# Performance work log

Hardware: AMD Instinct MI355X
Metric: run time of the kernel (lower is better)

The kernel has to match this reference:

```python
import jax, jax.numpy as jnp
import numpy as np
from jax import lax

NUM_CLASSES = 21      # VOC: background (class 0) + 20 fg classes
TOP_K = 200           # max detections kept per (image, class)
CONF_THRESH = 0.01
NMS_THRESH = 0.45
VAR0, VAR1 = 0.1, 0.2 # cfg.VARIANCE
K_PRE = 256           # candidates pre-selected per class before NMS (fixed-shape NMS)


def setup_inputs() -> dict:
    key = jax.random.key(0)
    k1, k2, k3 = jax.random.split(key, 3)
    B, P, C = 32, 8732, NUM_CLASSES
    loc_data = jax.random.normal(k1, (B, P, 4), dtype=jnp.float32)
    conf_data = jax.random.normal(k2, (B, P, C), dtype=jnp.float32)
    u = jax.random.uniform(k3, (P, 4), dtype=jnp.float32)
    # priors in center-offset form: centers in [0,1), w/h in [0.02, 0.32)
    prior_data = jnp.concatenate([u[:, :2], 0.02 + 0.3 * u[:, 2:]], axis=-1)
    return {"loc_data": loc_data, "conf_data": conf_data, "prior_data": prior_data}


def decode(loc, priors):
    # loc, priors: [..., 4]; priors are (cx, cy, w, h)
    centers = priors[..., :2] + loc[..., :2] * VAR0 * priors[..., 2:]
    wh = priors[..., 2:] * jnp.exp(loc[..., 2:] * VAR1)
    xy_min = centers - wh * 0.5
    return jnp.concatenate([xy_min, xy_min + wh], axis=-1)  # (x1,y1,x2,y2)


def pairwise_iou(b):
    # b: [K, 4] corner boxes -> [K, K] IoU
    area = jnp.maximum(b[:, 2] - b[:, 0], 0.0) * jnp.maximum(b[:, 3] - b[:, 1], 0.0)
    lt = jnp.maximum(b[:, None, :2], b[None, :, :2])
    rb = jnp.minimum(b[:, None, 2:], b[None, :, 2:])
    wh = jnp.clip(rb - lt, 0.0)
    inter = wh[..., 0] * wh[..., 1]
    union = area[:, None] + area[None, :] - inter
    return inter / jnp.maximum(union, 1e-9)


def nms_one_class(scores_p, boxes_p4):
    # scores_p: [P], boxes_p4: [P, 4]; fixed-shape NMS -> [TOP_K, 5] (score, x1, y1, x2, y2)
    vals, idx = lax.top_k(scores_p, K_PRE)          # sorted descending
    cand = boxes_p4[idx]                            # [K_PRE, 4]
    valid = vals > CONF_THRESH
    iou = pairwise_iou(cand)                        # [K_PRE, K_PRE]
    ar = jnp.arange(K_PRE)

    def step(keep, i):
        # a kept box suppresses later boxes overlapping it above threshold
        sup = keep[i] & (iou[i] > NMS_THRESH) & (ar > i)
        return keep & (~sup), None

    keep, _ = lax.scan(step, valid, ar)
    kept_scores = jnp.where(keep, vals, 0.0)
    # kept entries are already score-ordered; pull the top TOP_K survivors to the front
    sv, si = lax.top_k(kept_scores, TOP_K)
    out_boxes = jnp.where(sv[:, None] > 0.0, cand[si], 0.0)
    return jnp.concatenate([sv[:, None], out_boxes], axis=-1)  # [TOP_K, 5]


def reference(loc_data, conf_data, prior_data):
    # loc_data: [B, P, 4], conf_data: [B, P, C], prior_data: [P, 4]
    probs = jax.nn.softmax(conf_data, axis=-1)                     # [B, P, C]
    probs_fg = jnp.swapaxes(probs[..., 1:], 1, 2)                  # [B, C-1, P] (skip background)
    boxes = decode(loc_data, prior_data[None, :, :])               # [B, P, 4]
    # vmap over classes, then over batch
    per_class = jax.vmap(nms_one_class, in_axes=(0, None))         # ([C-1,P],[P,4]) -> [C-1,TOP_K,5]
    per_image = jax.vmap(per_class, in_axes=(0, 0))
    return per_image(probs_fg, boxes)                              # [B, C-1, TOP_K, 5]
```

## Files before the change

### kernel.cpp

```cpp
#include <hip/hip_runtime.h>
#include <stdint.h>

typedef unsigned long long ull;
typedef float f4v __attribute__((ext_vector_type(4)));

#define NUM_CLASSES 21
#define NFG 20
#define TOPK 200
#define KPRE 256
#define CONF_TH 0.01f
#define NMS_TH 0.45f
#define VAR0 0.1f
#define VAR1 0.2f
#define NVMAX 35
#define BITS_CONF 0x3C23D70Au
#define BSLOT(g) ((g) + ((g) >> 6))

__global__ __launch_bounds__(256) void softmax_probs_kernel(
    const float* __restrict__ conf, float* __restrict__ probs, int B, int P) {
    __shared__ __align__(16) float buf[256 * NUM_CLASSES];
    const int t = threadIdx.x;
    const int nch = (P + 255) >> 8;

    const int id = blockIdx.x;
    int b, chk;
    if ((B & 7) == 0) {
        int r = id & 7, m = id >> 3;
        int q = m / nch;
        b = r + (q << 3);
        chk = m - q * nch;
    } else {
        b = id / nch;
        chk = id - b * nch;
    }
    const int p0 = chk << 8;
    const int cnt = min(256, P - p0);
    const float* src = conf + ((size_t)b * P + p0) * NUM_CLASSES;

    if (cnt == 256) {
        const f4v* s4 = (const f4v*)src;
        f4v* b4 = (f4v*)buf;
#pragma unroll
        for (int k = 0; k < 6; ++k) {
            int i = (k << 8) + t;
            if (i < (256 * NUM_CLASSES) / 4)
                b4[i] = __builtin_nontemporal_load(s4 + i);
        }
    } else {
        int n = cnt * NUM_CLASSES;
        for (int i = t; i < n; i += 256) buf[i] = src[i];
    }
    __syncthreads();

    float sc[NFG];
    if (t < cnt) {
        const float* row = buf + t * NUM_CLASSES;
        float x[NUM_CLASSES];
        float mx = row[0];
        x[0] = mx;
#pragma unroll
        for (int j = 1; j < NUM_CLASSES; ++j) { x[j] = row[j]; mx = fmaxf(mx, x[j]); }
        float s = 0.f;
#pragma unroll
        for (int j = 0; j < NUM_CLASSES; ++j) { x[j] = expf(x[j] - mx); s += x[j]; }
#pragma unroll
        for (int c = 1; c < NUM_CLASSES; ++c)
            sc[c - 1] = x[c] / s;
    }
    __syncthreads();

    if (t < cnt) {
#pragma unroll
        for (int c = 0; c < NFG; ++c)
            buf[c * 256 + t] = sc[c];
    }
    __syncthreads();

    float* dst = probs + ((size_t)b * NFG) * P + p0;
    if (cnt == 256) {
#pragma unroll
        for (int k = 0; k < 5; ++k) {
            int e = (k << 8) + t;
            int c = e >> 6;
            int f = e & 63;
            f4v val = ((const f4v*)buf)[(c << 6) + f];
            __builtin_nontemporal_store(val, (f4v*)(dst + (size_t)c * P + (f << 2)));
        }
    } else {
        for (int e = t; e < NFG * cnt; e += 256) {
            int c = e / cnt;
            int f = e - c * cnt;
            __builtin_nontemporal_store(buf[c * 256 + f], dst + (size_t)c * P + f);
        }
    }
}

__global__ __launch_bounds__(KPRE) void nms_topk_kernel(
    const float* __restrict__ probs, const float* __restrict__ loc,
    const float* __restrict__ prior, float* __restrict__ out, int B, int P) {

    __shared__ ull arr[2 * KPRE];
    __shared__ ull arr2[2 * KPRE];
    __shared__ int wsum[2][4];
    __shared__ int s_cnt;
    __shared__ float4 sbox[KPRE + (KPRE >> 6)];
    __shared__ float sarea[KPRE + (KPRE >> 6)];
    __shared__ ull smask[KPRE][5];
    __shared__ ull kept_mask[4];

    const int t = threadIdx.x;
    const int lane = t & 63;
    const int wid = t >> 6;
    const ull lmask_lt = (1ULL << lane) - 1ULL;

    const int g = blockIdx.x;
    int b, c;
    if ((B & 7) == 0) {
        int k = g >> 3;
        b = ((k / NFG) << 3) + (g & 7);
        c = k - (k / NFG) * NFG;
    } else {
        b = g / NFG;
        c = g - (g / NFG) * NFG;
    }
    const int pair = b * NFG + c;
    const float* sp = probs + (size_t)pair * P;

    unsigned int ubits[NVMAX];
#pragma unroll
    for (int i = 0; i < NVMAX; ++i) {
        int p = (i << 8) + t;
        ubits[i] = (p < P) ? __float_as_uint(sp[p]) : 0u;
    }

    {
        unsigned int lo = 0x3C23u, hi = 0x3F81u;
        while (hi - lo > 1u) {
            unsigned int mid = lo + ((hi - lo) >> 1);
            unsigned int m32 = mid << 16;
            int cc = 0;
#pragma unroll
            for (int i = 0; i < NVMAX; ++i)
                cc += __popcll(__ballot(ubits[i] >= m32));
            if (cc >= KPRE / 4) lo = mid; else hi = mid;
        }
        if (lane == 0) wsum[0][wid] = (int)(lo << 16);
    }
    __syncthreads();
    unsigned int T = (unsigned int)min(min(wsum[0][0], wsum[0][1]),
                                       min(wsum[0][2], wsum[0][3]));

    int nval;
    for (int attempt = 0;; ++attempt) {
        if (t == 0) s_cnt = 0;
        __syncthreads();
        int wtot = 0;
#pragma unroll
        for (int i = 0; i < NVMAX; ++i) {
            int p = (i << 8) + t;
            bool pred = (p < P) && (ubits[i] >= T);
            wtot += __popcll(__ballot(pred));
        }
        int wbase = 0;
        if (lane == 0) wbase = atomicAdd(&s_cnt, wtot);
        wbase = __shfl(wbase, 0);
        int run = wbase;
#pragma unroll
        for (int i = 0; i < NVMAX; ++i) {
            int p = (i << 8) + t;
            bool pred = (p < P) && (ubits[i] >= T);
            ull bal = __ballot(pred);
            if (pred) {
                int slot = run + __popcll(bal & lmask_lt);
                if (slot < 2 * KPRE)
                    arr[slot] = ((ull)ubits[i] << 32) | (unsigned int)(~p);
            }
            run += __popcll(bal);
        }
        __syncthreads();
        if (s_cnt <= 2 * KPRE || attempt == 1) { nval = min(s_cnt, 2 * KPRE); break; }
        unsigned int lo = T, hi = 0x3F800001u;
        int it = 0;
        while (hi - lo > 1u) {
            unsigned int mid = lo + ((hi - lo) >> 1);
            int cc = 0;
#pragma unroll
            for (int i = 0; i < NVMAX; ++i)
                cc += __popcll(__ballot(ubits[i] >= mid));
            if (lane == 0) wsum[it & 1][wid] = cc;
            __syncthreads();
            int totc = wsum[it & 1][0] + wsum[it & 1][1] + wsum[it & 1][2] + wsum[it & 1][3];
            if (totc >= KPRE) lo = mid; else hi = mid;
            ++it;
        }
        T = lo;
    }

    for (int e = t; e < 2 * KPRE; e += KPRE)
        if (e >= nval) arr[e] = 0ULL;
    __syncthreads();

    ull k0 = arr[t];
    ull k1 = arr[t + KPRE];
    {
        int lstage = 0;
#pragma unroll
        for (int kk = 2; kk <= 2 * KPRE; kk <<= 1) {
#pragma unroll
            for (int j = kk >> 1; j > 0; j >>= 1) {
                if (j == KPRE) {
                    ull mx = (k0 > k1) ? k0 : k1;
                    ull mn = (k0 > k1) ? k1 : k0;
                    k0 = mx; k1 = mn;
                } else if (j >= 64) {
                    ull* A = (lstage & 1) ? arr : arr2;
                    ++lstage;
                    A[t] = k0; A[t + KPRE] = k1;
                    __syncthreads();
                    ull o0 = A[t ^ j];
                    ull o1 = A[(t + KPRE) ^ j];
                    bool amLow = ((t & j) == 0);
                    bool d0 = ((t & kk) == 0);
                    bool d1 = (((t + KPRE) & kk) == 0);
                    k0 = (d0 == amLow) ? ((k0 > o0) ? k0 : o0) : ((k0 > o0) ? o0 : k0);
                    k1 = (d1 == amLow) ? ((k1 > o1) ? k1 : o1) : ((k1 > o1) ? o1 : k1);
                } else {
                    ull o0 = __shfl_xor(k0, j);
                    ull o1 = __shfl_xor(k1, j);
                    bool amLow = ((t & j) == 0);
                    bool d0 = ((t & kk) == 0);
                    bool d1 = (((t + KPRE) & kk) == 0);
                    k0 = (d0 == amLow) ? ((k0 > o0) ? k0 : o0) : ((k0 > o0) ? o0 : k0);
                    k1 = (d1 == amLow) ? ((k1 > o1) ? k1 : o1) : ((k1 > o1) ? o1 : k1);
                }
            }
        }
    }
    const ull key = k0;

    float v = __uint_as_float((unsigned int)(key >> 32));
    int idx = (int)(~(unsigned int)(key & 0xFFFFFFFFu));
    if (idx < 0 || idx >= P) { idx = 0; v = 0.f; }

    const float4 lv = *(const float4*)(loc + ((size_t)b * P + idx) * 4);
    const float4 pv = *(const float4*)(prior + (size_t)idx * 4);
    float cx = pv.x + (lv.x * VAR0) * pv.z;
    float cy = pv.y + (lv.y * VAR0) * pv.w;
    float w = pv.z * expf(lv.z * VAR1);
    float h = pv.w * expf(lv.w * VAR1);
    float x1 = cx - w * 0.5f;
    float y1 = cy - h * 0.5f;
    float x2 = x1 + w;
    float y2 = y1 + h;
    float myarea = fmaxf(x2 - x1, 0.f) * fmaxf(y2 - y1, 0.f);

    sbox[BSLOT(t)] = make_float4(x1, y1, x2, y2);
    sarea[BSLOT(t)] = myarea;
    __syncthreads();

#pragma unroll
    for (int rep = 0; rep < 3; ++rep) {
        int pid = t + (rep << 8);
        if (pid < 640) {
            int r, w2;
            if (pid < 64)       { r = pid;                w2 = 0; }
            else if (pid < 192) { int q = pid - 64;  r = 64  + (q >> 1); w2 = q & 1; }
            else if (pid < 384) { int q = pid - 192; int q3 = q / 3; r = 128 + q3; w2 = q - 3 * q3; }
            else                { int q = pid - 384; r = 192 + (q >> 2); w2 = q & 3; }
            float4 rb = sbox[BSLOT(r)];
            float ra = sarea[BSLOT(r)];
            ull mm = 0ULL;
            for (int i = 0; i < 64; ++i) {
                int gg = (w2 << 6) + i;
                float4 gb = sbox[BSLOT(gg)];
                float lx = fmaxf(gb.x, rb.x), ly = fmaxf(gb.y, rb.y);
                float rx = fminf(gb.z, rb.z), ry = fminf(gb.w, rb.w);
                float iw = fmaxf(rx - lx, 0.f), ih = fmaxf(ry - ly, 0.f);
                float inter = iw * ih;
                float uni = sarea[BSLOT(gg)] + ra - inter;
                bool s = (inter / fmaxf(uni, 1e-9f)) > NMS_TH;
                mm |= ((ull)(s ? 1u : 0u)) << i;
            }
            smask[r][w2] = mm;
        }
    }
    __syncthreads();

    ull m0 = smask[t][0];
    ull m1 = (wid >= 1) ? smask[t][1] : 0ULL;
    ull m2 = (wid >= 2) ? smask[t][2] : 0ULL;
    ull m3 = (wid >= 3) ? smask[t][3] : 0ULL;
    if (wid == 0) m0 &= lmask_lt;
    else if (wid == 1) m1 &= lmask_lt;
    else if (wid == 2) m2 &= lmask_lt;
    else m3 &= lmask_lt;

    int alive = (v > CONF_TH) ? 1 : 0;
    ull mykept = 0ULL;
#pragma unroll
    for (int w2 = 0; w2 < 4; ++w2) {
        if (wid == w2) {
            if (w2 > 0 && (m0 & kept_mask[0])) alive = 0;
            if (w2 > 1 && (m1 & kept_mask[1])) alive = 0;
            if (w2 > 2 && (m2 & kept_mask[2])) alive = 0;
            ull mw = (w2 == 0) ? m0 : (w2 == 1) ? m1 : (w2 == 2) ? m2 : m3;
            ull validb = __ballot(alive != 0);
            ull todo = __ballot((mw & validb) != 0ULL) & validb;
            ull kept = validb & ~todo;
            while (todo) {
                int i = __builtin_ctzll(todo);
                ull row = __shfl(mw, i);
                if ((row & kept) == 0ULL) kept |= (1ULL << i);
                todo &= (todo - 1ULL);
            }
            mykept = kept;
            alive = (int)((kept >> lane) & 1ULL);
            if (lane == 0) kept_mask[w2] = kept;
        }
        __syncthreads();
    }

    int rank = 0;
#pragma unroll
    for (int w2 = 0; w2 < 4; ++w2)
        if (w2 < wid) rank += __popcll(kept_mask[w2]);
    rank += __popcll(mykept & lmask_lt);
    int total = 0;
#pragma unroll
    for (int w2 = 0; w2 < 4; ++w2) total += __popcll(kept_mask[w2]);

    float* orow = out + (size_t)pair * TOPK * 5;
    if (alive && rank < TOPK) {
        float* o = orow + rank * 5;
        o[0] = v; o[1] = x1; o[2] = y1; o[3] = x2; o[4] = y2;
    }
    if (t < TOPK && t >= total) {
        float* o = orow + t * 5;
        o[0] = 0.f; o[1] = 0.f; o[2] = 0.f; o[3] = 0.f; o[4] = 0.f;
    }
}

extern "C" void kernel_launch(void* const* d_in, const int* in_sizes, int n_in,
                              void* d_out, int out_size, void* d_ws, size_t ws_size,
                              hipStream_t stream) {
    const float* loc = (const float*)d_in[0];
    const float* conf = (const float*)d_in[1];
    const float* prior = (const float*)d_in[2];
    float* out = (float*)d_out;
    float* probs = (float*)d_ws;

    int P = in_sizes[2] / 4;
    int B = in_sizes[0] / (4 * P);
    int nch = (P + 255) / 256;

    softmax_probs_kernel<<<dim3(B * nch), 256, 0, stream>>>(conf, probs, B, P);
    nms_topk_kernel<<<B * NFG, KPRE, 0, stream>>>(probs, loc, prior, out, B, P);
}
```

Measured before the change: 130.4 us.

## Store truncated 16-bit probabilities and recompute exact scores for candidates only

```diff
diff --git a/kernel.cpp b/kernel.cpp
--- a/kernel.cpp
+++ b/kernel.cpp
@@ -12,13 +12,16 @@
 #define NMS_TH 0.45f
 #define VAR0 0.1f
 #define VAR1 0.2f
-#define NVMAX 35
-#define BITS_CONF 0x3C23D70Au
+#define NV16 18
+#define T16_LO 0x3C23u
+#define T16_HI 0x3F81u
 #define BSLOT(g) ((g) + ((g) >> 6))
 
-__global__ __launch_bounds__(256) void softmax_probs_kernel(
-    const float* __restrict__ conf, float* __restrict__ probs, int B, int P) {
+__global__ __launch_bounds__(256) void rownorm16_kernel(
+    const float* __restrict__ conf, float2* __restrict__ norm,
+    ushort* __restrict__ probs16, int B, int P) {
     __shared__ __align__(16) float buf[256 * NUM_CLASSES];
+    __shared__ __align__(16) ushort b16[NFG * 256];
     const int t = threadIdx.x;
     const int nch = (P + 255) >> 8;
 
@@ -43,8 +46,7 @@
 #pragma unroll
         for (int k = 0; k < 6; ++k) {
             int i = (k << 8) + t;
-            if (i < (256 * NUM_CLASSES) / 4)
-                b4[i] = __builtin_nontemporal_load(s4 + i);
+            if (i < (256 * NUM_CLASSES) / 4) b4[i] = s4[i];
         }
     } else {
         int n = cnt * NUM_CLASSES;
@@ -52,7 +54,6 @@
     }
     __syncthreads();
 
-    float sc[NFG];
     if (t < cnt) {
         const float* row = buf + t * NUM_CLASSES;
         float x[NUM_CLASSES];
@@ -63,40 +64,37 @@
         float s = 0.f;
 #pragma unroll
         for (int j = 0; j < NUM_CLASSES; ++j) { x[j] = expf(x[j] - mx); s += x[j]; }
-#pragma unroll
-        for (int c = 1; c < NUM_CLASSES; ++c)
-            sc[c - 1] = x[c] / s;
-    }
-    __syncthreads();
-
-    if (t < cnt) {
-#pragma unroll
-        for (int c = 0; c < NFG; ++c)
-            buf[c * 256 + t] = sc[c];
-    }
-    __syncthreads();
-
-    float* dst = probs + ((size_t)b * NFG) * P + p0;
+        norm[(size_t)b * P + p0 + t] = make_float2(mx, s);
+#pragma unroll
+        for (int c = 1; c < NUM_CLASSES; ++c) {
+            float v = x[c] / s;
+            b16[(c - 1) * 256 + t] = (ushort)(__float_as_uint(v) >> 16);
+        }
+    }
+    __syncthreads();
+
     if (cnt == 256) {
-#pragma unroll
-        for (int k = 0; k < 5; ++k) {
+        const uint* s32 = (const uint*)b16;
+#pragma unroll
+        for (int k = 0; k < 10; ++k) {
             int e = (k << 8) + t;
-            int c = e >> 6;
-            int f = e & 63;
-            f4v val = ((const f4v*)buf)[(c << 6) + f];
-            __builtin_nontemporal_store(val, (f4v*)(dst + (size_t)c * P + (f << 2)));
+            int c = e >> 7;
+            int q = e & 127;
+            uint* dstu = (uint*)(probs16 + ((size_t)b * NFG + c) * P + p0);
+            dstu[q] = s32[(c << 7) + q];
         }
     } else {
         for (int e = t; e < NFG * cnt; e += 256) {
             int c = e / cnt;
             int f = e - c * cnt;
-            __builtin_nontemporal_store(buf[c * 256 + f], dst + (size_t)c * P + f);
+            probs16[((size_t)b * NFG + c) * P + p0 + f] = b16[c * 256 + f];
         }
     }
 }
 
 __global__ __launch_bounds__(KPRE) void nms_topk_kernel(
-    const float* __restrict__ probs, const float* __restrict__ loc,
+    const float* __restrict__ conf, const float2* __restrict__ norm,
+    const ushort* __restrict__ probs16, const float* __restrict__ loc,
     const float* __restrict__ prior, float* __restrict__ out, int B, int P) {
 
     __shared__ ull arr[2 * KPRE];
@@ -124,31 +122,35 @@
         c = g - (g / NFG) * NFG;
     }
     const int pair = b * NFG + c;
-    const float* sp = probs + (size_t)pair * P;
-
-    unsigned int ubits[NVMAX];
-#pragma unroll
-    for (int i = 0; i < NVMAX; ++i) {
-        int p = (i << 8) + t;
-        ubits[i] = (p < P) ? __float_as_uint(sp[p]) : 0u;
-    }
-
+    const int nq = P >> 1;
+
+    unsigned int u2[NV16];
     {
-        unsigned int lo = 0x3C23u, hi = 0x3F81u;
+        const uint* sp16 = (const uint*)(probs16 + (size_t)pair * P);
+#pragma unroll
+        for (int i = 0; i < NV16; ++i) {
+            int q = (i << 8) + t;
+            u2[i] = (q < nq) ? sp16[q] : 0u;
+        }
+    }
+
+    {
+        unsigned int lo = T16_LO, hi = T16_HI;
         while (hi - lo > 1u) {
             unsigned int mid = lo + ((hi - lo) >> 1);
-            unsigned int m32 = mid << 16;
             int cc = 0;
 #pragma unroll
-            for (int i = 0; i < NVMAX; ++i)
-                cc += __popcll(__ballot(ubits[i] >= m32));
+            for (int i = 0; i < NV16; ++i) {
+                cc += __popcll(__ballot((u2[i] & 0xFFFFu) >= mid));
+                cc += __popcll(__ballot((u2[i] >> 16) >= mid));
+            }
             if (cc >= KPRE / 4) lo = mid; else hi = mid;
         }
-        if (lane == 0) wsum[0][wid] = (int)(lo << 16);
-    }
-    __syncthreads();
-    unsigned int T = (unsigned int)min(min(wsum[0][0], wsum[0][1]),
-                                       min(wsum[0][2], wsum[0][3]));
+        if (lane == 0) wsum[0][wid] = (int)lo;
+    }
+    __syncthreads();
+    unsigned int T16 = (unsigned int)min(min(wsum[0][0], wsum[0][1]),
+                                         min(wsum[0][2], wsum[0][3]));
 
     int nval;
     for (int attempt = 0;; ++attempt) {
@@ -156,52 +158,77 @@
         __syncthreads();
         int wtot = 0;
 #pragma unroll
-        for (int i = 0; i < NVMAX; ++i) {
-            int p = (i << 8) + t;
-            bool pred = (p < P) && (ubits[i] >= T);
-            wtot += __popcll(__ballot(pred));
+        for (int i = 0; i < NV16; ++i) {
+            wtot += __popcll(__ballot((u2[i] & 0xFFFFu) >= T16));
+            wtot += __popcll(__ballot((u2[i] >> 16) >= T16));
         }
         int wbase = 0;
         if (lane == 0) wbase = atomicAdd(&s_cnt, wtot);
         wbase = __shfl(wbase, 0);
         int run = wbase;
 #pragma unroll
-        for (int i = 0; i < NVMAX; ++i) {
-            int p = (i << 8) + t;
-            bool pred = (p < P) && (ubits[i] >= T);
-            ull bal = __ballot(pred);
-            if (pred) {
-                int slot = run + __popcll(bal & lmask_lt);
-                if (slot < 2 * KPRE)
-                    arr[slot] = ((ull)ubits[i] << 32) | (unsigned int)(~p);
-            }
-            run += __popcll(bal);
+        for (int i = 0; i < NV16; ++i) {
+#pragma unroll
+            for (int h = 0; h < 2; ++h) {
+                unsigned int bits16 = h ? (u2[i] >> 16) : (u2[i] & 0xFFFFu);
+                bool pred = (bits16 >= T16);
+                ull bal = __ballot(pred);
+                if (pred) {
+                    int slot = run + __popcll(bal & lmask_lt);
+                    if (slot < 2 * KPRE)
+                        arr[slot] = (ull)(unsigned int)((((i << 8) + t) << 1) + h);
+                }
+                run += __popcll(bal);
+            }
         }
         __syncthreads();
         if (s_cnt <= 2 * KPRE || attempt == 1) { nval = min(s_cnt, 2 * KPRE); break; }
-        unsigned int lo = T, hi = 0x3F800001u;
+        unsigned int lo = T16, hi = T16_HI;
         int it = 0;
         while (hi - lo > 1u) {
             unsigned int mid = lo + ((hi - lo) >> 1);
             int cc = 0;
 #pragma unroll
-            for (int i = 0; i < NVMAX; ++i)
-                cc += __popcll(__ballot(ubits[i] >= mid));
+            for (int i = 0; i < NV16; ++i) {
+                cc += __popcll(__ballot((u2[i] & 0xFFFFu) >= mid));
+                cc += __popcll(__ballot((u2[i] >> 16) >= mid));
+            }
             if (lane == 0) wsum[it & 1][wid] = cc;
             __syncthreads();
             int totc = wsum[it & 1][0] + wsum[it & 1][1] + wsum[it & 1][2] + wsum[it & 1][3];
             if (totc >= KPRE) lo = mid; else hi = mid;
             ++it;
         }
-        T = lo;
+        T16 = lo;
     }
 
     for (int e = t; e < 2 * KPRE; e += KPRE)
-        if (e >= nval) arr[e] = 0ULL;
-    __syncthreads();
-
-    ull k0 = arr[t];
-    ull k1 = arr[t + KPRE];
+        if (e >= nval) arr[e] = (ull)0xFFFFFFFFu;
+    __syncthreads();
+
+    const float* cb = conf + (size_t)b * P * NUM_CLASSES + (c + 1);
+    const float2* nb = norm + (size_t)b * P;
+    ull k0, k1;
+    {
+        unsigned int pa = (unsigned int)arr[t];
+        unsigned int pb2 = (unsigned int)arr[t + KPRE];
+        const bool va = (pa < (unsigned int)P);
+        const bool vb = (pb2 < (unsigned int)P);
+        float xa = 0.f, xb = 0.f;
+        float2 ma = make_float2(0.f, 1.f), mb = make_float2(0.f, 1.f);
+        if (va) { xa = cb[(size_t)pa * NUM_CLASSES]; ma = nb[pa]; }
+        if (vb) { xb = cb[(size_t)pb2 * NUM_CLASSES]; mb = nb[pb2]; }
+        if (va) {
+            float v = expf(xa - ma.x) / ma.y;
+            k0 = ((ull)__float_as_uint(v) << 32) | (unsigned int)(~pa);
+        } else k0 = 0ULL;
+        if (vb) {
+            float v = expf(xb - mb.x) / mb.y;
+            k1 = ((ull)__float_as_uint(v) << 32) | (unsigned int)(~pb2);
+        } else k1 = 0ULL;
+    }
+    __syncthreads();
+
     {
         int lstage = 0;
 #pragma unroll
@@ -347,12 +374,14 @@
     const float* conf = (const float*)d_in[1];
     const float* prior = (const float*)d_in[2];
     float* out = (float*)d_out;
-    float* probs = (float*)d_ws;
 
     int P = in_sizes[2] / 4;
     int B = in_sizes[0] / (4 * P);
     int nch = (P + 255) / 256;
 
-    softmax_probs_kernel<<<dim3(B * nch), 256, 0, stream>>>(conf, probs, B, P);
-    nms_topk_kernel<<<B * NFG, KPRE, 0, stream>>>(probs, loc, prior, out, B, P);
+    float2* norm = (float2*)d_ws;
+    ushort* probs16 = (ushort*)((char*)d_ws + (size_t)B * P * 8);
+
+    rownorm16_kernel<<<dim3(B * nch), 256, 0, stream>>>(conf, norm, probs16, B, P);
+    nms_topk_kernel<<<B * NFG, KPRE, 0, stream>>>(conf, norm, probs16, loc, prior, out, B, P);
 }
```

Measured after the change: 126.8 us. 1.03x faster.
